# Optimization experiments

Hardware: AMD Instinct MI355X
Metric: run time of the kernel (lower is better)

## Reference

```python
import jax, jax.numpy as jnp
import numpy as np

U = I = 4096; E = 128; K = 4; D = E // K; R = 3; B = 512; L = 100
LAMB = 0.5; L2NORM = 1e-4; EPS = 1e-8


def _l2norm(x, axis):
    n = jnp.sqrt(jnp.sum(x * x, axis=axis, keepdims=True))
    return x / jnp.maximum(n, 1e-12)


def setup_inputs() -> dict:
    key = jax.random.key(0)
    ks = jax.random.split(key, 16)
    def adj(k, shape, p=0.01):
        return jax.random.bernoulli(k, p, shape).astype(jnp.float32)
    relation_mats = adj(ks[0], (R, U, I))
    item_graphs = adj(ks[1], (R, I, I))
    train_matrix = relation_mats[0]
    inp = {
        "user": jax.random.randint(ks[2], (B, 1), 0, U),
        "item": jax.random.randint(ks[3], (B, L), 0, I),
        "user_embedding": jax.random.normal(ks[4], (U, E), jnp.float32) * 0.1,
        "item_embedding": jax.random.normal(ks[5], (I, E), jnp.float32) * 0.1,
        "mgnn_weight": jax.random.normal(ks[6], (R,), jnp.float32),
        "item_behaviour_W": jax.random.normal(ks[7], (R, E, E), jnp.float32) * 0.05,
        "item_propagate_W": jax.random.normal(ks[8], (R, E, E), jnp.float32) * 0.05,
        "W": jax.random.normal(ks[9], (E, E), jnp.float32) * 0.05,
        "W_K": jax.random.normal(ks[10], (K, D, E), jnp.float32) * 0.05,
        "B_K": jax.random.normal(ks[11], (K, D), jnp.float32) * 0.05,
        "train_matrix": train_matrix,
        "relation_mats": relation_mats,
        "item_graphs": item_graphs,
        "item_graph_degree": item_graphs.sum(axis=2, keepdims=True),  # [R,I,1]
        "user_behaviour_degree": relation_mats.sum(axis=2).T,  # [U,R]
    }
    return inp


def reference(user, item, user_embedding, item_embedding, mgnn_weight,
              item_behaviour_W, item_propagate_W, W, W_K, B_K,
              train_matrix, relation_mats, item_graphs, item_graph_degree,
              user_behaviour_degree):
    # behaviour weighting: [U,R]
    total_weight = user_behaviour_degree @ mgnn_weight[:, None]  # [U,1]
    ubw = user_behaviour_degree * mgnn_weight[None, :] / (total_weight + EPS)

    # K-head projections (relation-independent; original recomputes identically per relation)
    s_i = _l2norm(jax.nn.relu(jnp.einsum('kde,ie->kdi', W_K, item_embedding) + B_K[..., None]), axis=1)  # [K,D,I]
    s_u0 = _l2norm(jax.nn.relu(jnp.einsum('kde,ue->kdu', W_K, user_embedding) + B_K[..., None]), axis=1)  # [K,D,U]
    s_u0 = jnp.transpose(s_u0, (2, 0, 1))  # [U,K,D]

    ue_blocks = user_embedding.reshape(U, K, D)
    logits = jnp.einsum('ukd,kdi->kui', ue_blocks, s_i)  # [K,U,I]
    r = jax.nn.softmax(logits, axis=0)  # exp / sum over K heads

    user_feature = jnp.zeros((U, E), user_embedding.dtype)
    score2 = jnp.zeros((B, L), user_embedding.dtype)
    for i in range(R):
        rel = relation_mats[i]  # [U,I]
        # item-item propagation
        tip = ((item_graphs[i] @ item_embedding) / (item_graph_degree[i] + EPS)) @ item_propagate_W[i]  # [I,E]
        tmp_item_emb = tip[item]  # [B,L,E]
        # attention-weighted user-item propagation per head
        s_u = s_u0 + jnp.einsum('kui,kdi->ukd', r * rel[None], s_i)  # [U,K,D]
        tun = _l2norm(s_u, axis=2).reshape(U, E)  # tmp_user_neighbour
        tuinp = (rel @ tip) / (user_behaviour_degree[:, i:i + 1] + EPS)  # [U,E]
        user_feature = user_feature + ubw[:, i:i + 1] * tun
        proj = tuinp @ item_behaviour_W[i]  # [U,E]
        score2 = score2 + jnp.sum(proj[user[:, 0]][:, None, :] * tmp_item_emb, axis=2)
    score2 = score2 / R

    item_feature = (train_matrix.T @ user_embedding) @ W  # [I,E]
    user_feature = user_feature @ W  # [U,E]

    uf = user_feature[user[:, 0]][:, None, :]  # [B,1,E]
    itf = item_feature[item]  # [B,L,E]
    score1 = jnp.sum(uf * itf, axis=2)  # [B,L]
    scores = score1 + LAMB * score2
    L2_loss = L2NORM * (L * jnp.sum(uf ** 2) + jnp.sum(itf ** 2))
    return scores, L2_loss
```

## Files before the change

### kernel.cpp

```cpp
#include <hip/hip_runtime.h>

#define NU 4096
#define NI 4096
#define NR 3
#define NB 512
#define NL 100
#define FEPS 1e-8f

#define WS_SI    0
#define WS_EMBW  524288
#define WS_TIP   2097152
#define WS_UEW   3670016
#define WS_ITEMF 4194304
#define WS_WTUN  4718592
#define WS_PROJ  4915200
#define WS_UF    5111808
#define WS_UF2P  5177344
#define WS_ITF2P 5177856
#define WS_BMT   5190656
#define WS_GBITS 5714944

__global__ void k_stream(const float* __restrict__ iemb, const float* __restrict__ ipW,
                         const float* __restrict__ uemb, const float* __restrict__ Wm,
                         const float* __restrict__ WK, const float* __restrict__ BK,
                         const float* __restrict__ tm, const float* __restrict__ G,
                         float* __restrict__ embW, float* __restrict__ uew,
                         float* __restrict__ si,
                         unsigned long long* __restrict__ bmT,
                         unsigned long long* __restrict__ gbits) {
  int t = threadIdx.x;
  int bid = blockIdx.x;
  if (bid < 16384) {
    __shared__ unsigned char nib[4][256];
    const float* src = (bid < NU) ? (tm + (size_t)bid * NI)
                                  : (G + (size_t)(bid - NU) * NI);
    const float4* r4 = (const float4*)src;
#pragma unroll
    for (int q = 0; q < 4; ++q) {
      float4 v = r4[q * 256 + t];
      unsigned m = 0;
      if (v.x != 0.f) m |= 1u;
      if (v.y != 0.f) m |= 2u;
      if (v.z != 0.f) m |= 4u;
      if (v.w != 0.f) m |= 8u;
      nib[q][t] = (unsigned char)m;
    }
    __syncthreads();
    if (t < 64) {
      unsigned long long mm = 0;
#pragma unroll
      for (int j = 0; j < 16; ++j) {
        int e = t * 16 + j;
        mm |= (unsigned long long)nib[e >> 8][e & 255] << (4 * j);
      }
      if (bid < NU) bmT[(size_t)t * NU + bid] = mm;
      else gbits[(size_t)(bid - NU) * 64 + t] = mm;
    }
  } else if (bid < 17408) {
    __shared__ __align__(16) float shbuf[2048];
    int lb = bid - 16384;
    int batch = lb >> 8, rb = lb & 255;
    const float* in;
    const float* Wp;
    float* out;
    if (batch < 3) {
      in = iemb;
      Wp = ipW + (size_t)batch * 16384;
      out = embW + (size_t)batch * NI * 128;
    } else {
      in = uemb; Wp = Wm; out = uew;
    }
    const float4* in4 = (const float4*)(in + (size_t)rb * 2048);
    for (int c = t; c < 512; c += 256) ((float4*)shbuf)[c] = in4[c];
    __syncthreads();
    int c = t & 127, g = t >> 7;
    float acc[8];
#pragma unroll
    for (int rr = 0; rr < 8; ++rr) acc[rr] = 0.f;
    for (int e = 0; e < 128; ++e) {
      float wv = Wp[e * 128 + c];
#pragma unroll
      for (int rr = 0; rr < 8; ++rr) acc[rr] += shbuf[(g * 8 + rr) * 128 + e] * wv;
    }
#pragma unroll
    for (int rr = 0; rr < 8; ++rr) out[((size_t)rb * 16 + g * 8 + rr) * 128 + c] = acc[rr];
  } else {
    __shared__ __align__(16) float embs2[256];
    int tl = t & 127, half = t >> 7;
    int item = (bid - 17408) * 2 + half;
    float* embs = embs2 + half * 128;
    if (tl < 32) ((float4*)embs)[tl] = ((const float4*)(iemb + (size_t)item * 128))[tl];
    __syncthreads();
    float acc = BK[tl];
    const float4* wk4 = (const float4*)(WK + (size_t)tl * 128);
    const float4* e4 = (const float4*)embs;
#pragma unroll 8
    for (int c = 0; c < 32; ++c) {
      float4 w = wk4[c], v = e4[c];
      acc += w.x * v.x + w.y * v.y + w.z * v.z + w.w * v.w;
    }
    acc = fmaxf(acc, 0.f);
    float sq = acc * acc;
#pragma unroll
    for (int m = 1; m <= 16; m <<= 1) sq += __shfl_xor(sq, m);
    si[(size_t)item * 128 + tl] = acc / fmaxf(sqrtf(sq), 1e-12f);
  }
}

__global__ void k_gather(const unsigned long long* __restrict__ gbits,
                         const unsigned long long* __restrict__ bmT,
                         const float* __restrict__ embW, const float* __restrict__ uew,
                         const float* __restrict__ deg,
                         float* __restrict__ tip, float* __restrict__ itemf) {
  int t = threadIdx.x;
  int bid = blockIdx.x;
  if (bid < 12288) {
    int r = bid >> 12;
    __shared__ int nz[512];
    __shared__ int cnt;
    __shared__ float4 red[8][32];
    if (t == 0) cnt = 0;
    __syncthreads();
    if (t < 64) {
      unsigned long long m = gbits[(size_t)bid * 64 + t];
      int base = t * 64;
      while (m) {
        int b = __ffsll(m) - 1;
        m &= m - 1;
        nz[atomicAdd(&cnt, 1)] = base + b;
      }
    }
    __syncthreads();
    int n = min(cnt, 512);
    int g = t >> 5, f = t & 31;
    float4 acc = {0.f, 0.f, 0.f, 0.f};
    const float4* e4 = (const float4*)(embW + (size_t)r * NI * 128);
    for (int p = g; p < n; p += 8) {
      float4 v = e4[(size_t)nz[p] * 32 + f];
      acc.x += v.x; acc.y += v.y; acc.z += v.z; acc.w += v.w;
    }
    red[g][f] = acc;
    __syncthreads();
    if (t < 32) {
      float4 s = red[0][t];
#pragma unroll
      for (int q = 1; q < 8; ++q) {
        float4 v = red[q][t];
        s.x += v.x; s.y += v.y; s.z += v.z; s.w += v.w;
      }
      float inv = 1.f / (deg[bid] + FEPS);
      s.x *= inv; s.y *= inv; s.z *= inv; s.w *= inv;
      ((float4*)(tip + (size_t)bid * 128))[t] = s;
    }
  } else {
    int i = bid - 12288;
    int ct = i >> 6;
    unsigned long long bitm = 1ull << (i & 63);
    __shared__ int lst[192];
    __shared__ int cnt2;
    __shared__ float red2[3][128];
    if (t == 0) cnt2 = 0;
    __syncthreads();
    const unsigned long long* col = bmT + (size_t)ct * NU;
#pragma unroll
    for (int cc = 0; cc < 16; ++cc) {
      unsigned long long m = col[cc * 256 + t];
      if (m & bitm) lst[atomicAdd(&cnt2, 1)] = cc * 256 + t;
    }
    __syncthreads();
    int n = min(cnt2, 192);
    int w = t >> 6, l = t & 63;
    float ax = 0.f, ay = 0.f;
    const float2* uew2 = (const float2*)uew;
    for (int p = w; p < n; p += 4) {
      float2 v = uew2[(size_t)lst[p] * 64 + l];
      ax += v.x; ay += v.y;
    }
    if (w > 0) { red2[w - 1][2 * l] = ax; red2[w - 1][2 * l + 1] = ay; }
    __syncthreads();
    if (w == 0) {
      float2 o;
      o.x = ax + red2[0][2 * l] + red2[1][2 * l] + red2[2][2 * l];
      o.y = ay + red2[0][2 * l + 1] + red2[1][2 * l + 1] + red2[2][2 * l + 1];
      ((float2*)(itemf + (size_t)i * 128))[l] = o;
    }
  }
}

__global__ void k_user(const int* __restrict__ user, const float* __restrict__ relm,
                       const float* __restrict__ si, const float* __restrict__ tip,
                       const float* __restrict__ uemb, const float* __restrict__ WK,
                       const float* __restrict__ BK, const float* __restrict__ ibW,
                       const float* __restrict__ ubd, const float* __restrict__ mw,
                       float* __restrict__ wtun, float* __restrict__ proj) {
  int bid = blockIdx.x;
  int r = bid >> 9, b = bid & 511;
  int u = user[b];
  const float* rel = relm + ((size_t)r * NU + u) * NI;
  __shared__ int nz[512];
  __shared__ int cnt;
  __shared__ __align__(16) float uel[128];
  __shared__ float redA[4][128];
  __shared__ float redB[4][128];
  __shared__ float tu[128];
  int t = threadIdx.x;
  if (t == 0) cnt = 0;
  if (t < 32) ((float4*)uel)[t] = ((const float4*)(uemb + (size_t)u * 128))[t];
  __syncthreads();
  const float4* rel4 = (const float4*)rel;
#pragma unroll
  for (int c = 0; c < 4; ++c) {
    int idx4 = c * 256 + t;
    float4 v = rel4[idx4];
    int j0 = idx4 << 2;
    if (v.x != 0.f) nz[atomicAdd(&cnt, 1)] = j0;
    if (v.y != 0.f) nz[atomicAdd(&cnt, 1)] = j0 + 1;
    if (v.z != 0.f) nz[atomicAdd(&cnt, 1)] = j0 + 2;
    if (v.w != 0.f) nz[atomicAdd(&cnt, 1)] = j0 + 3;
  }
  __syncthreads();
  int n = min(cnt, 512);
  int wid = t >> 6, lane = t & 63;
  int k = lane >> 4;
  float2 myue = ((const float2*)uel)[lane];
  float sux = 0.f, suy = 0.f, tpx = 0.f, tpy = 0.f;
  const float2* si2 = (const float2*)si;
  const float2* tip2 = (const float2*)(tip + (size_t)r * NI * 128);
  for (int p = wid; p < n; p += 4) {
    int i = nz[p];
    float2 sv = si2[(size_t)i * 64 + lane];
    float lg = myue.x * sv.x + myue.y * sv.y;
    lg += __shfl_xor(lg, 1);
    lg += __shfl_xor(lg, 2);
    lg += __shfl_xor(lg, 4);
    lg += __shfl_xor(lg, 8);
    float l0 = __shfl(lg, 0), l1 = __shfl(lg, 16), l2 = __shfl(lg, 32), l3 = __shfl(lg, 48);
    float mx = fmaxf(fmaxf(l0, l1), fmaxf(l2, l3));
    float e0 = __expf(l0 - mx), e1 = __expf(l1 - mx), e2 = __expf(l2 - mx), e3 = __expf(l3 - mx);
    float inv = 1.f / (e0 + e1 + e2 + e3);
    float myr = (k == 0 ? e0 : k == 1 ? e1 : k == 2 ? e2 : e3) * inv;
    sux += myr * sv.x;
    suy += myr * sv.y;
    float2 tv = tip2[(size_t)i * 64 + lane];
    tpx += tv.x;
    tpy += tv.y;
  }
  redA[wid][2 * lane] = sux; redA[wid][2 * lane + 1] = suy;
  redB[wid][2 * lane] = tpx; redB[wid][2 * lane + 1] = tpy;
  __syncthreads();
  if (t < 128) {
    float suv = redA[0][t] + redA[1][t] + redA[2][t] + redA[3][t];
    float tipv = redB[0][t] + redB[1][t] + redB[2][t] + redB[3][t];
    float a = BK[t];
    const float4* wk4 = (const float4*)(WK + (size_t)t * 128);
    const float4* ue4 = (const float4*)uel;
#pragma unroll 8
    for (int c = 0; c < 32; ++c) {
      float4 w = wk4[c], v = ue4[c];
      a += w.x * v.x + w.y * v.y + w.z * v.z + w.w * v.w;
    }
    a = fmaxf(a, 0.f);
    float sq = a * a;
#pragma unroll
    for (int m = 1; m <= 16; m <<= 1) sq += __shfl_xor(sq, m);
    float su = a / fmaxf(sqrtf(sq), 1e-12f) + suv;
    float sq2 = su * su;
#pragma unroll
    for (int m = 1; m <= 16; m <<= 1) sq2 += __shfl_xor(sq2, m);
    float tun = su / fmaxf(sqrtf(sq2), 1e-12f);
    float d0 = ubd[u * 3], d1 = ubd[u * 3 + 1], d2 = ubd[u * 3 + 2];
    float w0 = mw[0], w1 = mw[1], w2 = mw[2];
    float tw = d0 * w0 + d1 * w1 + d2 * w2;
    float dr = (r == 0 ? d0 : r == 1 ? d1 : d2);
    float wr = (r == 0 ? w0 : r == 1 ? w1 : w2);
    wtun[(size_t)(b * 3 + r) * 128 + t] = (dr * wr / (tw + FEPS)) * tun;
    tu[t] = tipv / (dr + FEPS);
  }
  __syncthreads();
  int ep = t & 127, hh = t >> 7;
  const float* Wb = ibW + (size_t)r * 16384;
  float pacc = 0.f;
  for (int e = hh * 64; e < hh * 64 + 64; ++e) pacc += tu[e] * Wb[e * 128 + ep];
  redA[hh][ep] = pacc;
  __syncthreads();
  if (hh == 0) proj[(size_t)(b * 3 + r) * 128 + ep] = redA[0][ep] + redA[1][ep];
}

__global__ void k_uf(const float* __restrict__ wtun, const float* __restrict__ Wm,
                     float* __restrict__ uf, float* __restrict__ uf2p) {
  int b = blockIdx.x, t = threadIdx.x;
  __shared__ float comb[128];
  __shared__ float part[2];
  comb[t] = wtun[(size_t)(b * 3) * 128 + t] + wtun[(size_t)(b * 3 + 1) * 128 + t] +
            wtun[(size_t)(b * 3 + 2) * 128 + t];
  __syncthreads();
  float acc = 0.f;
  for (int e = 0; e < 128; ++e) acc += comb[e] * Wm[e * 128 + t];
  uf[(size_t)b * 128 + t] = acc;
  float sq = acc * acc;
#pragma unroll
  for (int m = 1; m <= 32; m <<= 1) sq += __shfl_xor(sq, m);
  if ((t & 63) == 0) part[t >> 6] = sq;
  __syncthreads();
  if (t == 0) uf2p[b] = part[0] + part[1];
}

__global__ void k_score(const int* __restrict__ item, const float* __restrict__ itemf,
                        const float* __restrict__ uf, const float* __restrict__ tip,
                        const float* __restrict__ proj, float* __restrict__ out,
                        float* __restrict__ itf2p) {
  int t = threadIdx.x, wid = t >> 6, lane = t & 63;
  int idx = blockIdx.x * 4 + wid;
  int b = idx / NL;
  int it = item[idx];
  float2 av = ((const float2*)(itemf + (size_t)it * 128))[lane];
  float2 cv = ((const float2*)(uf + (size_t)b * 128))[lane];
  float s1 = av.x * cv.x + av.y * cv.y;
  float sqi = av.x * av.x + av.y * av.y;
  float s2 = 0.f;
#pragma unroll
  for (int r = 0; r < 3; ++r) {
    float2 tv = ((const float2*)(tip + ((size_t)r * NI + it) * 128))[lane];
    float2 pv = ((const float2*)(proj + (size_t)(b * 3 + r) * 128))[lane];
    s2 += tv.x * pv.x + tv.y * pv.y;
  }
#pragma unroll
  for (int m = 1; m <= 32; m <<= 1) {
    s1 += __shfl_xor(s1, m);
    s2 += __shfl_xor(s2, m);
    sqi += __shfl_xor(sqi, m);
  }
  if (lane == 0) out[idx] = s1 + 0.5f * (s2 * (1.f / 3.f));
  __shared__ float sh[4];
  if (lane == 0) sh[wid] = sqi;
  __syncthreads();
  if (t == 0) itf2p[blockIdx.x] = sh[0] + sh[1] + sh[2] + sh[3];
}

__global__ void k_final(const float* __restrict__ itf2p, const float* __restrict__ uf2p,
                        float* __restrict__ out) {
  int t = threadIdx.x;
  float v = 0.f;
  for (int i = t; i < 12800; i += 256) v += itf2p[i];
  float vu = 0.f;
  for (int i = t; i < NB; i += 256) vu += uf2p[i];
  v += 100.f * vu;
#pragma unroll
  for (int m = 1; m <= 32; m <<= 1) v += __shfl_xor(v, m);
  __shared__ float sh[4];
  if ((t & 63) == 0) sh[t >> 6] = v;
  __syncthreads();
  if (t == 0) out[NB * NL] = 1e-4f * (sh[0] + sh[1] + sh[2] + sh[3]);
}

extern "C" void kernel_launch(void* const* d_in, const int* in_sizes, int n_in,
                              void* d_out, int out_size, void* d_ws, size_t ws_size,
                              hipStream_t stream) {
  (void)in_sizes; (void)n_in; (void)out_size; (void)ws_size;
  const int* user = (const int*)d_in[0];
  const int* item = (const int*)d_in[1];
  const float* uemb = (const float*)d_in[2];
  const float* iemb = (const float*)d_in[3];
  const float* mw = (const float*)d_in[4];
  const float* ibW = (const float*)d_in[5];
  const float* ipW = (const float*)d_in[6];
  const float* Wm = (const float*)d_in[7];
  const float* WK = (const float*)d_in[8];
  const float* BK = (const float*)d_in[9];
  const float* tm = (const float*)d_in[10];
  const float* relm = (const float*)d_in[11];
  const float* ig = (const float*)d_in[12];
  const float* igd = (const float*)d_in[13];
  const float* ubd = (const float*)d_in[14];
  float* out = (float*)d_out;
  float* ws = (float*)d_ws;
  unsigned long long* bmT = (unsigned long long*)(ws + WS_BMT);
  unsigned long long* gbits = (unsigned long long*)(ws + WS_GBITS);

  k_stream<<<19456, 256, 0, stream>>>(iemb, ipW, uemb, Wm, WK, BK, tm, ig,
                                      ws + WS_EMBW, ws + WS_UEW, ws + WS_SI, bmT, gbits);
  k_gather<<<16384, 256, 0, stream>>>(gbits, bmT, ws + WS_EMBW, ws + WS_UEW, igd,
                                      ws + WS_TIP, ws + WS_ITEMF);
  k_user<<<NR * NB, 256, 0, stream>>>(user, relm, ws + WS_SI, ws + WS_TIP, uemb, WK, BK,
                                      ibW, ubd, mw, ws + WS_WTUN, ws + WS_PROJ);
  k_uf<<<NB, 128, 0, stream>>>(ws + WS_WTUN, Wm, ws + WS_UF, ws + WS_UF2P);
  k_score<<<12800, 256, 0, stream>>>(item, ws + WS_ITEMF, ws + WS_UF, ws + WS_TIP,
                                     ws + WS_PROJ, out, ws + WS_ITF2P);
  k_final<<<1, 256, 0, stream>>>(ws + WS_ITF2P, ws + WS_UF2P, out);
}
```

Measured before the change: 189.0 us.

## Split dense-to-bitmask scan into wave-ballot kernel with interleaved bit layout

Replaces the per-row shared-memory nibble packing of the adjacency matrices with a separate grid-stride kernel in which each wave uses ballot instructions to build 64-bit masks directly. This changes the bit layout to an interleaved column order, so the gather kernel's index decoding and column selection are updated to match. The small matmul part becomes its own kernel and now stages the weight matrix in shared memory in chunks. The aim is to cut shared-memory traffic and instruction count in the bandwidth-bound scan, at the cost of an extra kernel launch and more complex index arithmetic.

```diff
diff --git a/kernel.cpp b/kernel.cpp
--- a/kernel.cpp
+++ b/kernel.cpp
@@ -20,46 +20,66 @@
 #define WS_BMT   5190656
 #define WS_GBITS 5714944
 
-__global__ void k_stream(const float* __restrict__ iemb, const float* __restrict__ ipW,
+
+__global__ void k_scan2(const float* __restrict__ tm, const float* __restrict__ G,
+                        unsigned long long* __restrict__ bmT,
+                        unsigned long long* __restrict__ gbits) {
+  int wid = (blockIdx.x << 2) + (threadIdx.x >> 6);
+  int lane = threadIdx.x & 63;
+  for (int task = wid; task < 65536; task += 8192) {
+    int row = task >> 2;
+    int cq = (task & 3) << 2;
+    const float* src = (row < NU) ? (tm + (size_t)row * NI)
+                                  : (G + (size_t)(row - NU) * NI);
+    const float4* s4 = (const float4*)src + (cq << 6) + lane;
+    float4 v0 = s4[0];
+    float4 v1 = s4[64];
+    float4 v2 = s4[128];
+    float4 v3 = s4[192];
+    unsigned long long a0 = __ballot(v0.x != 0.f), a1 = __ballot(v0.y != 0.f),
+                       a2 = __ballot(v0.z != 0.f), a3 = __ballot(v0.w != 0.f);
+    unsigned long long b0 = __ballot(v1.x != 0.f), b1 = __ballot(v1.y != 0.f),
+                       b2 = __ballot(v1.z != 0.f), b3 = __ballot(v1.w != 0.f);
+    unsigned long long c0 = __ballot(v2.x != 0.f), c1 = __ballot(v2.y != 0.f),
+                       c2 = __ballot(v2.z != 0.f), c3 = __ballot(v2.w != 0.f);
+    unsigned long long d0 = __ballot(v3.x != 0.f), d1 = __ballot(v3.y != 0.f),
+                       d2 = __ballot(v3.z != 0.f), d3 = __ballot(v3.w != 0.f);
+    if (lane == 0) {
+      if (row < NU) {
+        size_t base = ((size_t)cq << 14) + row;
+        bmT[base] = a0;                bmT[base + (1 << 12)] = a1;
+        bmT[base + (2 << 12)] = a2;    bmT[base + (3 << 12)] = a3;
+        size_t b1b = base + (1 << 14);
+        bmT[b1b] = b0;                 bmT[b1b + (1 << 12)] = b1;
+        bmT[b1b + (2 << 12)] = b2;     bmT[b1b + (3 << 12)] = b3;
+        size_t b2b = base + (2 << 14);
+        bmT[b2b] = c0;                 bmT[b2b + (1 << 12)] = c1;
+        bmT[b2b + (2 << 12)] = c2;     bmT[b2b + (3 << 12)] = c3;
+        size_t b3b = base + (3 << 14);
+        bmT[b3b] = d0;                 bmT[b3b + (1 << 12)] = d1;
+        bmT[b3b + (2 << 12)] = d2;     bmT[b3b + (3 << 12)] = d3;
+      } else {
+        unsigned long long* g = gbits + (((size_t)(row - NU)) << 6) + (cq << 2);
+        g[0] = a0;  g[1] = a1;  g[2] = a2;  g[3] = a3;
+        g[4] = b0;  g[5] = b1;  g[6] = b2;  g[7] = b3;
+        g[8] = c0;  g[9] = c1;  g[10] = c2; g[11] = c3;
+        g[12] = d0; g[13] = d1; g[14] = d2; g[15] = d3;
+      }
+    }
+  }
+}
+
+__global__ void k_bmm_si(const float* __restrict__ iemb, const float* __restrict__ ipW,
                          const float* __restrict__ uemb, const float* __restrict__ Wm,
                          const float* __restrict__ WK, const float* __restrict__ BK,
-                         const float* __restrict__ tm, const float* __restrict__ G,
                          float* __restrict__ embW, float* __restrict__ uew,
-                         float* __restrict__ si,
-                         unsigned long long* __restrict__ bmT,
-                         unsigned long long* __restrict__ gbits) {
+                         float* __restrict__ si) {
   int t = threadIdx.x;
   int bid = blockIdx.x;
-  if (bid < 16384) {
-    __shared__ unsigned char nib[4][256];
-    const float* src = (bid < NU) ? (tm + (size_t)bid * NI)
-                                  : (G + (size_t)(bid - NU) * NI);
-    const float4* r4 = (const float4*)src;
-#pragma unroll
-    for (int q = 0; q < 4; ++q) {
-      float4 v = r4[q * 256 + t];
-      unsigned m = 0;
-      if (v.x != 0.f) m |= 1u;
-      if (v.y != 0.f) m |= 2u;
-      if (v.z != 0.f) m |= 4u;
-      if (v.w != 0.f) m |= 8u;
-      nib[q][t] = (unsigned char)m;
-    }
-    __syncthreads();
-    if (t < 64) {
-      unsigned long long mm = 0;
-#pragma unroll
-      for (int j = 0; j < 16; ++j) {
-        int e = t * 16 + j;
-        mm |= (unsigned long long)nib[e >> 8][e & 255] << (4 * j);
-      }
-      if (bid < NU) bmT[(size_t)t * NU + bid] = mm;
-      else gbits[(size_t)(bid - NU) * 64 + t] = mm;
-    }
-  } else if (bid < 17408) {
-    __shared__ __align__(16) float shbuf[2048];
-    int lb = bid - 16384;
-    int batch = lb >> 8, rb = lb & 255;
+  if (bid < 1024) {
+    __shared__ __align__(16) float inl[16][128];
+    __shared__ __align__(16) float wt[32][128];
+    int batch = bid >> 8, rb = bid & 255;
     const float* in;
     const float* Wp;
     float* out;
@@ -71,23 +91,30 @@
       in = uemb; Wp = Wm; out = uew;
     }
     const float4* in4 = (const float4*)(in + (size_t)rb * 2048);
-    for (int c = t; c < 512; c += 256) ((float4*)shbuf)[c] = in4[c];
-    __syncthreads();
+    for (int c = t; c < 512; c += 256) ((float4*)inl)[c] = in4[c];
     int c = t & 127, g = t >> 7;
     float acc[8];
 #pragma unroll
     for (int rr = 0; rr < 8; ++rr) acc[rr] = 0.f;
-    for (int e = 0; e < 128; ++e) {
-      float wv = Wp[e * 128 + c];
-#pragma unroll
-      for (int rr = 0; rr < 8; ++rr) acc[rr] += shbuf[(g * 8 + rr) * 128 + e] * wv;
+    const float4* Wp4 = (const float4*)Wp;
+    for (int p = 0; p < 4; ++p) {
+      __syncthreads();
+#pragma unroll
+      for (int j = 0; j < 4; ++j) ((float4*)wt)[j * 256 + t] = Wp4[p * 1024 + j * 256 + t];
+      __syncthreads();
+      int e0 = p * 32;
+      for (int e2 = 0; e2 < 32; ++e2) {
+        float wv = wt[e2][c];
+#pragma unroll
+        for (int rr = 0; rr < 8; ++rr) acc[rr] += inl[g * 8 + rr][e0 + e2] * wv;
+      }
     }
 #pragma unroll
     for (int rr = 0; rr < 8; ++rr) out[((size_t)rb * 16 + g * 8 + rr) * 128 + c] = acc[rr];
   } else {
     __shared__ __align__(16) float embs2[256];
     int tl = t & 127, half = t >> 7;
-    int item = (bid - 17408) * 2 + half;
+    int item = (bid - 1024) * 2 + half;
     float* embs = embs2 + half * 128;
     if (tl < 32) ((float4*)embs)[tl] = ((const float4*)(iemb + (size_t)item * 128))[tl];
     __syncthreads();
@@ -95,8 +122,8 @@
     const float4* wk4 = (const float4*)(WK + (size_t)tl * 128);
     const float4* e4 = (const float4*)embs;
 #pragma unroll 8
-    for (int c = 0; c < 32; ++c) {
-      float4 w = wk4[c], v = e4[c];
+    for (int cc = 0; cc < 32; ++cc) {
+      float4 w = wk4[cc], v = e4[cc];
       acc += w.x * v.x + w.y * v.y + w.z * v.z + w.w * v.w;
     }
     acc = fmaxf(acc, 0.f);
@@ -123,11 +150,11 @@
     __syncthreads();
     if (t < 64) {
       unsigned long long m = gbits[(size_t)bid * 64 + t];
-      int base = t * 64;
+      int base = ((t >> 2) << 8) + (t & 3);
       while (m) {
         int b = __ffsll(m) - 1;
         m &= m - 1;
-        nz[atomicAdd(&cnt, 1)] = base + b;
+        nz[atomicAdd(&cnt, 1)] = base + (b << 2);
       }
     }
     __syncthreads();
@@ -154,14 +181,14 @@
     }
   } else {
     int i = bid - 12288;
-    int ct = i >> 6;
-    unsigned long long bitm = 1ull << (i & 63);
+    int chunk = i >> 8, w8 = i & 255, q = w8 & 3, l = w8 >> 2;
+    unsigned long long bitm = 1ull << l;
     __shared__ int lst[192];
     __shared__ int cnt2;
     __shared__ float red2[3][128];
     if (t == 0) cnt2 = 0;
     __syncthreads();
-    const unsigned long long* col = bmT + (size_t)ct * NU;
+    const unsigned long long* col = bmT + (((size_t)(chunk << 2) + q) << 12);
 #pragma unroll
     for (int cc = 0; cc < 16; ++cc) {
       unsigned long long m = col[cc * 256 + t];
@@ -169,20 +196,20 @@
     }
     __syncthreads();
     int n = min(cnt2, 192);
-    int w = t >> 6, l = t & 63;
+    int w = t >> 6, l2 = t & 63;
     float ax = 0.f, ay = 0.f;
     const float2* uew2 = (const float2*)uew;
     for (int p = w; p < n; p += 4) {
-      float2 v = uew2[(size_t)lst[p] * 64 + l];
+      float2 v = uew2[(size_t)lst[p] * 64 + l2];
       ax += v.x; ay += v.y;
     }
-    if (w > 0) { red2[w - 1][2 * l] = ax; red2[w - 1][2 * l + 1] = ay; }
+    if (w > 0) { red2[w - 1][2 * l2] = ax; red2[w - 1][2 * l2 + 1] = ay; }
     __syncthreads();
     if (w == 0) {
       float2 o;
-      o.x = ax + red2[0][2 * l] + red2[1][2 * l] + red2[2][2 * l];
-      o.y = ay + red2[0][2 * l + 1] + red2[1][2 * l + 1] + red2[2][2 * l + 1];
-      ((float2*)(itemf + (size_t)i * 128))[l] = o;
+      o.x = ax + red2[0][2 * l2] + red2[1][2 * l2] + red2[2][2 * l2];
+      o.y = ay + red2[0][2 * l2 + 1] + red2[1][2 * l2 + 1] + red2[2][2 * l2 + 1];
+      ((float2*)(itemf + (size_t)i * 128))[l2] = o;
     }
   }
 }
@@ -377,8 +404,9 @@
   unsigned long long* bmT = (unsigned long long*)(ws + WS_BMT);
   unsigned long long* gbits = (unsigned long long*)(ws + WS_GBITS);
 
-  k_stream<<<19456, 256, 0, stream>>>(iemb, ipW, uemb, Wm, WK, BK, tm, ig,
-                                      ws + WS_EMBW, ws + WS_UEW, ws + WS_SI, bmT, gbits);
+  k_scan2<<<2048, 256, 0, stream>>>(tm, ig, bmT, gbits);
+  k_bmm_si<<<3072, 256, 0, stream>>>(iemb, ipW, uemb, Wm, WK, BK,
+                                     ws + WS_EMBW, ws + WS_UEW, ws + WS_SI);
   k_gather<<<16384, 256, 0, stream>>>(gbits, bmT, ws + WS_EMBW, ws + WS_UEW, igd,
                                       ws + WS_TIP, ws + WS_ITEMF);
   k_user<<<NR * NB, 256, 0, stream>>>(user, relm, ws + WS_SI, ws + WS_TIP, uemb, WK, BK,
```

Result: slower. 202.5 us (+7.2%).

## Scan item graphs directly in tip kernel and fuse user and uf kernels

Applied to the files above, without the earlier changes.

The item-graph bitmask pass is removed from the streaming kernel. The tip gather kernel now reads each dense item-graph row with nontemporal loads and builds its nonzero list in place, which drops one write and read round trip of the bitmask and shrinks the prep grid. The per-relation user kernel and the uf kernel are merged into one block per batch user that loops over the three relations and accumulates the weighted neighbour feature in shared memory, so the wtun buffer and one launch go away. In exchange, the user kernel now runs only 512 blocks doing serial relation work, which lowers parallelism, and the graph scan moves onto the critical path of the gather kernel.

```diff
diff --git a/kernel.cpp b/kernel.cpp
--- a/kernel.cpp
+++ b/kernel.cpp
@@ -7,37 +7,33 @@
 #define NL 100
 #define FEPS 1e-8f
 
+typedef float nf4 __attribute__((ext_vector_type(4)));
+
 #define WS_SI    0
 #define WS_EMBW  524288
 #define WS_TIP   2097152
 #define WS_UEW   3670016
 #define WS_ITEMF 4194304
-#define WS_WTUN  4718592
 #define WS_PROJ  4915200
 #define WS_UF    5111808
 #define WS_UF2P  5177344
 #define WS_ITF2P 5177856
 #define WS_BMT   5190656
-#define WS_GBITS 5714944
-
-__global__ void k_stream(const float* __restrict__ iemb, const float* __restrict__ ipW,
-                         const float* __restrict__ uemb, const float* __restrict__ Wm,
-                         const float* __restrict__ WK, const float* __restrict__ BK,
-                         const float* __restrict__ tm, const float* __restrict__ G,
-                         float* __restrict__ embW, float* __restrict__ uew,
-                         float* __restrict__ si,
-                         unsigned long long* __restrict__ bmT,
-                         unsigned long long* __restrict__ gbits) {
+
+__global__ void k_prep(const float* __restrict__ iemb, const float* __restrict__ ipW,
+                       const float* __restrict__ uemb, const float* __restrict__ Wm,
+                       const float* __restrict__ WK, const float* __restrict__ BK,
+                       const float* __restrict__ tm,
+                       float* __restrict__ embW, float* __restrict__ uew,
+                       float* __restrict__ si, unsigned long long* __restrict__ bmT) {
   int t = threadIdx.x;
   int bid = blockIdx.x;
-  if (bid < 16384) {
+  if (bid < 4096) {
     __shared__ unsigned char nib[4][256];
-    const float* src = (bid < NU) ? (tm + (size_t)bid * NI)
-                                  : (G + (size_t)(bid - NU) * NI);
-    const float4* r4 = (const float4*)src;
+    const nf4* r4 = (const nf4*)(tm + (size_t)bid * NI);
 #pragma unroll
     for (int q = 0; q < 4; ++q) {
-      float4 v = r4[q * 256 + t];
+      nf4 v = __builtin_nontemporal_load(&r4[q * 256 + t]);
       unsigned m = 0;
       if (v.x != 0.f) m |= 1u;
       if (v.y != 0.f) m |= 2u;
@@ -53,12 +49,11 @@
         int e = t * 16 + j;
         mm |= (unsigned long long)nib[e >> 8][e & 255] << (4 * j);
       }
-      if (bid < NU) bmT[(size_t)t * NU + bid] = mm;
-      else gbits[(size_t)(bid - NU) * 64 + t] = mm;
-    }
-  } else if (bid < 17408) {
+      bmT[(size_t)t * NU + bid] = mm;
+    }
+  } else if (bid < 5120) {
     __shared__ __align__(16) float shbuf[2048];
-    int lb = bid - 16384;
+    int lb = bid - 4096;
     int batch = lb >> 8, rb = lb & 255;
     const float* in;
     const float* Wp;
@@ -87,7 +82,7 @@
   } else {
     __shared__ __align__(16) float embs2[256];
     int tl = t & 127, half = t >> 7;
-    int item = (bid - 17408) * 2 + half;
+    int item = (bid - 5120) * 2 + half;
     float* embs = embs2 + half * 128;
     if (tl < 32) ((float4*)embs)[tl] = ((const float4*)(iemb + (size_t)item * 128))[tl];
     __syncthreads();
@@ -95,8 +90,8 @@
     const float4* wk4 = (const float4*)(WK + (size_t)tl * 128);
     const float4* e4 = (const float4*)embs;
 #pragma unroll 8
-    for (int c = 0; c < 32; ++c) {
-      float4 w = wk4[c], v = e4[c];
+    for (int cc = 0; cc < 32; ++cc) {
+      float4 w = wk4[cc], v = e4[cc];
       acc += w.x * v.x + w.y * v.y + w.z * v.z + w.w * v.w;
     }
     acc = fmaxf(acc, 0.f);
@@ -107,28 +102,30 @@
   }
 }
 
-__global__ void k_gather(const unsigned long long* __restrict__ gbits,
-                         const unsigned long long* __restrict__ bmT,
-                         const float* __restrict__ embW, const float* __restrict__ uew,
-                         const float* __restrict__ deg,
-                         float* __restrict__ tip, float* __restrict__ itemf) {
+__global__ void k_tipf(const float* __restrict__ G, const float* __restrict__ deg,
+                       const float* __restrict__ embW,
+                       const unsigned long long* __restrict__ bmT,
+                       const float* __restrict__ uew,
+                       float* __restrict__ tip, float* __restrict__ itemf) {
   int t = threadIdx.x;
   int bid = blockIdx.x;
   if (bid < 12288) {
     int r = bid >> 12;
+    const nf4* row4 = (const nf4*)(G + (size_t)bid * NI);
     __shared__ int nz[512];
     __shared__ int cnt;
     __shared__ float4 red[8][32];
     if (t == 0) cnt = 0;
     __syncthreads();
-    if (t < 64) {
-      unsigned long long m = gbits[(size_t)bid * 64 + t];
-      int base = t * 64;
-      while (m) {
-        int b = __ffsll(m) - 1;
-        m &= m - 1;
-        nz[atomicAdd(&cnt, 1)] = base + b;
-      }
+#pragma unroll
+    for (int c = 0; c < 4; ++c) {
+      int idx4 = c * 256 + t;
+      nf4 v = __builtin_nontemporal_load(&row4[idx4]);
+      int j0 = idx4 << 2;
+      if (v.x != 0.f) nz[atomicAdd(&cnt, 1)] = j0;
+      if (v.y != 0.f) nz[atomicAdd(&cnt, 1)] = j0 + 1;
+      if (v.z != 0.f) nz[atomicAdd(&cnt, 1)] = j0 + 2;
+      if (v.w != 0.f) nz[atomicAdd(&cnt, 1)] = j0 + 3;
     }
     __syncthreads();
     int n = min(cnt, 512);
@@ -187,70 +184,29 @@
   }
 }
 
-__global__ void k_user(const int* __restrict__ user, const float* __restrict__ relm,
-                       const float* __restrict__ si, const float* __restrict__ tip,
-                       const float* __restrict__ uemb, const float* __restrict__ WK,
-                       const float* __restrict__ BK, const float* __restrict__ ibW,
-                       const float* __restrict__ ubd, const float* __restrict__ mw,
-                       float* __restrict__ wtun, float* __restrict__ proj) {
-  int bid = blockIdx.x;
-  int r = bid >> 9, b = bid & 511;
+__global__ void k_user2(const int* __restrict__ user, const float* __restrict__ relm,
+                        const float* __restrict__ si, const float* __restrict__ tip,
+                        const float* __restrict__ uemb, const float* __restrict__ WK,
+                        const float* __restrict__ BK, const float* __restrict__ ibW,
+                        const float* __restrict__ ubd, const float* __restrict__ mw,
+                        const float* __restrict__ Wm,
+                        float* __restrict__ proj, float* __restrict__ uf,
+                        float* __restrict__ uf2p) {
+  int b = blockIdx.x;
+  int t = threadIdx.x;
   int u = user[b];
-  const float* rel = relm + ((size_t)r * NU + u) * NI;
   __shared__ int nz[512];
   __shared__ int cnt;
   __shared__ __align__(16) float uel[128];
+  __shared__ float su0[128];
+  __shared__ float comb[128];
+  __shared__ float tu[128];
   __shared__ float redA[4][128];
   __shared__ float redB[4][128];
-  __shared__ float tu[128];
-  int t = threadIdx.x;
-  if (t == 0) cnt = 0;
+  __shared__ float part[2];
   if (t < 32) ((float4*)uel)[t] = ((const float4*)(uemb + (size_t)u * 128))[t];
   __syncthreads();
-  const float4* rel4 = (const float4*)rel;
-#pragma unroll
-  for (int c = 0; c < 4; ++c) {
-    int idx4 = c * 256 + t;
-    float4 v = rel4[idx4];
-    int j0 = idx4 << 2;
-    if (v.x != 0.f) nz[atomicAdd(&cnt, 1)] = j0;
-    if (v.y != 0.f) nz[atomicAdd(&cnt, 1)] = j0 + 1;
-    if (v.z != 0.f) nz[atomicAdd(&cnt, 1)] = j0 + 2;
-    if (v.w != 0.f) nz[atomicAdd(&cnt, 1)] = j0 + 3;
-  }
-  __syncthreads();
-  int n = min(cnt, 512);
-  int wid = t >> 6, lane = t & 63;
-  int k = lane >> 4;
-  float2 myue = ((const float2*)uel)[lane];
-  float sux = 0.f, suy = 0.f, tpx = 0.f, tpy = 0.f;
-  const float2* si2 = (const float2*)si;
-  const float2* tip2 = (const float2*)(tip + (size_t)r * NI * 128);
-  for (int p = wid; p < n; p += 4) {
-    int i = nz[p];
-    float2 sv = si2[(size_t)i * 64 + lane];
-    float lg = myue.x * sv.x + myue.y * sv.y;
-    lg += __shfl_xor(lg, 1);
-    lg += __shfl_xor(lg, 2);
-    lg += __shfl_xor(lg, 4);
-    lg += __shfl_xor(lg, 8);
-    float l0 = __shfl(lg, 0), l1 = __shfl(lg, 16), l2 = __shfl(lg, 32), l3 = __shfl(lg, 48);
-    float mx = fmaxf(fmaxf(l0, l1), fmaxf(l2, l3));
-    float e0 = __expf(l0 - mx), e1 = __expf(l1 - mx), e2 = __expf(l2 - mx), e3 = __expf(l3 - mx);
-    float inv = 1.f / (e0 + e1 + e2 + e3);
-    float myr = (k == 0 ? e0 : k == 1 ? e1 : k == 2 ? e2 : e3) * inv;
-    sux += myr * sv.x;
-    suy += myr * sv.y;
-    float2 tv = tip2[(size_t)i * 64 + lane];
-    tpx += tv.x;
-    tpy += tv.y;
-  }
-  redA[wid][2 * lane] = sux; redA[wid][2 * lane + 1] = suy;
-  redB[wid][2 * lane] = tpx; redB[wid][2 * lane + 1] = tpy;
-  __syncthreads();
   if (t < 128) {
-    float suv = redA[0][t] + redA[1][t] + redA[2][t] + redA[3][t];
-    float tipv = redB[0][t] + redB[1][t] + redB[2][t] + redB[3][t];
     float a = BK[t];
     const float4* wk4 = (const float4*)(WK + (size_t)t * 128);
     const float4* ue4 = (const float4*)uel;
@@ -263,44 +219,88 @@
     float sq = a * a;
 #pragma unroll
     for (int m = 1; m <= 16; m <<= 1) sq += __shfl_xor(sq, m);
-    float su = a / fmaxf(sqrtf(sq), 1e-12f) + suv;
-    float sq2 = su * su;
-#pragma unroll
-    for (int m = 1; m <= 16; m <<= 1) sq2 += __shfl_xor(sq2, m);
-    float tun = su / fmaxf(sqrtf(sq2), 1e-12f);
-    float d0 = ubd[u * 3], d1 = ubd[u * 3 + 1], d2 = ubd[u * 3 + 2];
-    float w0 = mw[0], w1 = mw[1], w2 = mw[2];
-    float tw = d0 * w0 + d1 * w1 + d2 * w2;
-    float dr = (r == 0 ? d0 : r == 1 ? d1 : d2);
-    float wr = (r == 0 ? w0 : r == 1 ? w1 : w2);
-    wtun[(size_t)(b * 3 + r) * 128 + t] = (dr * wr / (tw + FEPS)) * tun;
-    tu[t] = tipv / (dr + FEPS);
-  }
-  __syncthreads();
-  int ep = t & 127, hh = t >> 7;
-  const float* Wb = ibW + (size_t)r * 16384;
-  float pacc = 0.f;
-  for (int e = hh * 64; e < hh * 64 + 64; ++e) pacc += tu[e] * Wb[e * 128 + ep];
-  redA[hh][ep] = pacc;
-  __syncthreads();
-  if (hh == 0) proj[(size_t)(b * 3 + r) * 128 + ep] = redA[0][ep] + redA[1][ep];
-}
-
-__global__ void k_uf(const float* __restrict__ wtun, const float* __restrict__ Wm,
-                     float* __restrict__ uf, float* __restrict__ uf2p) {
-  int b = blockIdx.x, t = threadIdx.x;
-  __shared__ float comb[128];
-  __shared__ float part[2];
-  comb[t] = wtun[(size_t)(b * 3) * 128 + t] + wtun[(size_t)(b * 3 + 1) * 128 + t] +
-            wtun[(size_t)(b * 3 + 2) * 128 + t];
-  __syncthreads();
-  float acc = 0.f;
-  for (int e = 0; e < 128; ++e) acc += comb[e] * Wm[e * 128 + t];
-  uf[(size_t)b * 128 + t] = acc;
-  float sq = acc * acc;
-#pragma unroll
-  for (int m = 1; m <= 32; m <<= 1) sq += __shfl_xor(sq, m);
-  if ((t & 63) == 0) part[t >> 6] = sq;
+    su0[t] = a / fmaxf(sqrtf(sq), 1e-12f);
+    comb[t] = 0.f;
+  }
+  float d0 = ubd[u * 3], d1 = ubd[u * 3 + 1], d2 = ubd[u * 3 + 2];
+  float w0 = mw[0], w1 = mw[1], w2 = mw[2];
+  float tw = d0 * w0 + d1 * w1 + d2 * w2;
+  int wid = t >> 6, lane = t & 63;
+  int k = lane >> 4;
+  const float2* si2 = (const float2*)si;
+  for (int r = 0; r < 3; ++r) {
+    if (t == 0) cnt = 0;
+    __syncthreads();
+    const nf4* rel4 = (const nf4*)(relm + ((size_t)r * NU + u) * NI);
+#pragma unroll
+    for (int c = 0; c < 4; ++c) {
+      int idx4 = c * 256 + t;
+      nf4 v = __builtin_nontemporal_load(&rel4[idx4]);
+      int j0 = idx4 << 2;
+      if (v.x != 0.f) nz[atomicAdd(&cnt, 1)] = j0;
+      if (v.y != 0.f) nz[atomicAdd(&cnt, 1)] = j0 + 1;
+      if (v.z != 0.f) nz[atomicAdd(&cnt, 1)] = j0 + 2;
+      if (v.w != 0.f) nz[atomicAdd(&cnt, 1)] = j0 + 3;
+    }
+    __syncthreads();
+    int n = min(cnt, 512);
+    float2 myue = ((const float2*)uel)[lane];
+    float sux = 0.f, suy = 0.f, tpx = 0.f, tpy = 0.f;
+    const float2* tip2 = (const float2*)(tip + (size_t)r * NI * 128);
+    for (int p = wid; p < n; p += 4) {
+      int i = nz[p];
+      float2 sv = si2[(size_t)i * 64 + lane];
+      float lg = myue.x * sv.x + myue.y * sv.y;
+      lg += __shfl_xor(lg, 1);
+      lg += __shfl_xor(lg, 2);
+      lg += __shfl_xor(lg, 4);
+      lg += __shfl_xor(lg, 8);
+      float l0 = __shfl(lg, 0), l1 = __shfl(lg, 16), l2 = __shfl(lg, 32), l3 = __shfl(lg, 48);
+      float mx = fmaxf(fmaxf(l0, l1), fmaxf(l2, l3));
+      float e0 = __expf(l0 - mx), e1 = __expf(l1 - mx), e2 = __expf(l2 - mx), e3 = __expf(l3 - mx);
+      float inv = 1.f / (e0 + e1 + e2 + e3);
+      float myr = (k == 0 ? e0 : k == 1 ? e1 : k == 2 ? e2 : e3) * inv;
+      sux += myr * sv.x;
+      suy += myr * sv.y;
+      float2 tv = tip2[(size_t)i * 64 + lane];
+      tpx += tv.x;
+      tpy += tv.y;
+    }
+    redA[wid][2 * lane] = sux; redA[wid][2 * lane + 1] = suy;
+    redB[wid][2 * lane] = tpx; redB[wid][2 * lane + 1] = tpy;
+    __syncthreads();
+    if (t < 128) {
+      float suv = redA[0][t] + redA[1][t] + redA[2][t] + redA[3][t];
+      float tipv = redB[0][t] + redB[1][t] + redB[2][t] + redB[3][t];
+      float su = su0[t] + suv;
+      float sq2 = su * su;
+#pragma unroll
+      for (int m = 1; m <= 16; m <<= 1) sq2 += __shfl_xor(sq2, m);
+      float tun = su / fmaxf(sqrtf(sq2), 1e-12f);
+      float dr = (r == 0 ? d0 : r == 1 ? d1 : d2);
+      float wr = (r == 0 ? w0 : r == 1 ? w1 : w2);
+      comb[t] += (dr * wr / (tw + FEPS)) * tun;
+      tu[t] = tipv / (dr + FEPS);
+    }
+    __syncthreads();
+    int ep = t & 127, hh = t >> 7;
+    const float* Wb = ibW + (size_t)r * 16384;
+    float pacc = 0.f;
+    for (int e = hh * 64; e < hh * 64 + 64; ++e) pacc += tu[e] * Wb[e * 128 + ep];
+    redA[hh][ep] = pacc;
+    __syncthreads();
+    if (hh == 0) proj[(size_t)(b * 3 + r) * 128 + ep] = redA[0][ep] + redA[1][ep];
+    __syncthreads();
+  }
+  if (t < 128) {
+    float acc = 0.f;
+    for (int e = 0; e < 128; ++e) acc += comb[e] * Wm[e * 128 + t];
+    uf[(size_t)b * 128 + t] = acc;
+    float sq = acc * acc;
+#pragma unroll
+    for (int m = 1; m <= 32; m <<= 1) sq += __shfl_xor(sq, m);
+    if ((t & 63) == 0) part[t >> 6] = sq;
+  }
   __syncthreads();
   if (t == 0) uf2p[b] = part[0] + part[1];
 }
@@ -375,15 +375,14 @@
   float* out = (float*)d_out;
   float* ws = (float*)d_ws;
   unsigned long long* bmT = (unsigned long long*)(ws + WS_BMT);
-  unsigned long long* gbits = (unsigned long long*)(ws + WS_GBITS);
-
-  k_stream<<<19456, 256, 0, stream>>>(iemb, ipW, uemb, Wm, WK, BK, tm, ig,
-                                      ws + WS_EMBW, ws + WS_UEW, ws + WS_SI, bmT, gbits);
-  k_gather<<<16384, 256, 0, stream>>>(gbits, bmT, ws + WS_EMBW, ws + WS_UEW, igd,
-                                      ws + WS_TIP, ws + WS_ITEMF);
-  k_user<<<NR * NB, 256, 0, stream>>>(user, relm, ws + WS_SI, ws + WS_TIP, uemb, WK, BK,
-                                      ibW, ubd, mw, ws + WS_WTUN, ws + WS_PROJ);
-  k_uf<<<NB, 128, 0, stream>>>(ws + WS_WTUN, Wm, ws + WS_UF, ws + WS_UF2P);
+
+  k_prep<<<7168, 256, 0, stream>>>(iemb, ipW, uemb, Wm, WK, BK, tm,
+                                   ws + WS_EMBW, ws + WS_UEW, ws + WS_SI, bmT);
+  k_tipf<<<16384, 256, 0, stream>>>(ig, igd, ws + WS_EMBW, bmT, ws + WS_UEW,
+                                    ws + WS_TIP, ws + WS_ITEMF);
+  k_user2<<<NB, 256, 0, stream>>>(user, relm, ws + WS_SI, ws + WS_TIP, uemb, WK, BK,
+                                  ibW, ubd, mw, Wm, ws + WS_PROJ, ws + WS_UF,
+                                  ws + WS_UF2P);
   k_score<<<12800, 256, 0, stream>>>(item, ws + WS_ITEMF, ws + WS_UF, ws + WS_TIP,
                                      ws + WS_PROJ, out, ws + WS_ITF2P);
   k_final<<<1, 256, 0, stream>>>(ws + WS_ITF2P, ws + WS_UF2P, out);
```

Result: slower. 205.2 us (+8.6%).
